# Kernel optimization log

Hardware: AMD Instinct MI355X
Metric: run time of the kernel (lower is better)

Reference implementation:

```python
import jax, jax.numpy as jnp
import numpy as np

D_MODEL = 1024
N_HEADS = 16
HEAD_DIM = D_MODEL // N_HEADS
D_FF = 4096
LN_EPS = 1e-5


def setup_inputs() -> dict:
    key = jax.random.key(0)
    ks = jax.random.split(key, 13)
    s = lambda fan_in: 1.0 / np.sqrt(fan_in)
    return {
        "x": jax.random.normal(ks[0], (2, 2048, D_MODEL), dtype=jnp.float32),
        "w_qkv": jax.random.uniform(ks[1], (D_MODEL, 3 * D_MODEL), jnp.float32, -s(D_MODEL), s(D_MODEL)),
        "b_qkv": jax.random.uniform(ks[2], (3 * D_MODEL,), jnp.float32, -s(D_MODEL), s(D_MODEL)),
        "w_out": jax.random.uniform(ks[3], (D_MODEL, D_MODEL), jnp.float32, -s(D_MODEL), s(D_MODEL)),
        "b_out": jax.random.uniform(ks[4], (D_MODEL,), jnp.float32, -s(D_MODEL), s(D_MODEL)),
        "w_ff1": jax.random.uniform(ks[5], (D_MODEL, D_FF), jnp.float32, -s(D_MODEL), s(D_MODEL)),
        "b_ff1": jax.random.uniform(ks[6], (D_FF,), jnp.float32, -s(D_MODEL), s(D_MODEL)),
        "w_ff2": jax.random.uniform(ks[7], (D_FF, D_MODEL), jnp.float32, -s(D_FF), s(D_FF)),
        "b_ff2": jax.random.uniform(ks[8], (D_MODEL,), jnp.float32, -s(D_FF), s(D_FF)),
        "ln1_g": jnp.ones((D_MODEL,), jnp.float32),
        "ln1_b": jnp.zeros((D_MODEL,), jnp.float32),
        "ln2_g": jnp.ones((D_MODEL,), jnp.float32),
        "ln2_b": jnp.zeros((D_MODEL,), jnp.float32),
    }


def _layer_norm(x, g, b):
    mu = jnp.mean(x, axis=-1, keepdims=True)
    var = jnp.mean(jnp.square(x - mu), axis=-1, keepdims=True)
    return (x - mu) * jax.lax.rsqrt(var + LN_EPS) * g + b


def reference(x, w_qkv, b_qkv, w_out, b_out, w_ff1, b_ff1, w_ff2, b_ff2,
              ln1_g, ln1_b, ln2_g, ln2_b):
    B, S, D = x.shape
    scale = HEAD_DIM ** -0.5
    qkv = x @ w_qkv + b_qkv                                   # [B,S,3D]
    qkv = qkv.reshape(B, S, 3, N_HEADS, HEAD_DIM)
    q, k, v = (qkv[:, :, 0], qkv[:, :, 1], qkv[:, :, 2])      # [B,S,H,Dh]
    attn = jnp.einsum("bqhd,bkhd->bhqk", q, k) * scale        # [B,H,S,S]
    attn = jax.nn.softmax(attn, axis=-1)
    o = jnp.einsum("bhqk,bkhd->bqhd", attn, v).reshape(B, S, D)
    o = o @ w_out + b_out
    x = _layer_norm(x + o, ln1_g, ln1_b)
    # FFN: Linear -> exact GELU -> Linear (dropout = 0)
    h = jax.nn.gelu(x @ w_ff1 + b_ff1, approximate=False)
    ff = h @ w_ff2 + b_ff2
    x = _layer_norm(x + ff, ln2_g, ln2_b)
    return x
```

## Files before the change

kernel.cpp:

```cpp
#include <hip/hip_runtime.h>
#include <hip/hip_bf16.h>
#include <cstdint>
#include <cstddef>

using bf16 = __hip_bfloat16;
typedef __attribute__((ext_vector_type(8))) short bf16x8;
typedef __attribute__((ext_vector_type(4))) float f32x4;

#define TOKENS 4096
#define DMODEL 1024
#define DFF    4096
#define SEQ    2048
#define NHEAD  16
#define HDIM   64
#define KVBLK  64
#define NT     (SEQ / KVBLK)
#define QSCALE 0.1803368801111f

__device__ __forceinline__ void async16(const void* g, void* l) {
  __builtin_amdgcn_global_load_lds(
      (const __attribute__((address_space(1))) void*)g,
      (__attribute__((address_space(3))) void*)l, 16, 0, 0);
}

__device__ __forceinline__ f32x4 mfma16(bf16x8 a, bf16x8 b, f32x4 c) {
  return __builtin_amdgcn_mfma_f32_16x16x32_bf16(a, b, c, 0, 0, 0);
}

__device__ __forceinline__ float exp2_fast(float x) {
  float r;
  asm("v_exp_f32 %0, %1" : "=v"(r) : "v"(x));
  return r;
}

__global__ void cast_bf16_k(const float* __restrict__ src, bf16* __restrict__ dst, int n) {
  int i = (blockIdx.x * blockDim.x + threadIdx.x) * 4;
  if (i >= n) return;
  float4 v = *(const float4*)(src + i);
  dst[i + 0] = __float2bfloat16(v.x);
  dst[i + 1] = __float2bfloat16(v.y);
  dst[i + 2] = __float2bfloat16(v.z);
  dst[i + 3] = __float2bfloat16(v.w);
}

__global__ void transpose_cast_k(const float* __restrict__ src, bf16* __restrict__ dst,
                                 int K, int N) {
  __shared__ float tile[32][33];
  int nt = blockIdx.x * 32, kt = blockIdx.y * 32;
  int tx = threadIdx.x, ty = threadIdx.y;
  #pragma unroll
  for (int i = 0; i < 32; i += 8)
    tile[ty + i][tx] = src[(size_t)(kt + ty + i) * N + nt + tx];
  __syncthreads();
  #pragma unroll
  for (int i = 0; i < 32; i += 8)
    dst[(size_t)(nt + ty + i) * K + kt + tx] = __float2bfloat16(tile[tx][ty + i]);
}

template <int EPI, int BN>
__global__ __launch_bounds__(256, 2)
void gemm_bt(const bf16* __restrict__ A, const bf16* __restrict__ Bt,
             const float* __restrict__ bias, int M, int N, int K,
             float* __restrict__ outf, bf16* __restrict__ outb,
             const float* __restrict__ resid,
             bf16* __restrict__ Qb, bf16* __restrict__ Kb, bf16* __restrict__ Vtb) {
  constexpr int MR = (BN == 128) ? 4 : 2;
  __shared__ bf16 Al[3][128 * 32];
  __shared__ bf16 Bl[3][BN * 32];
  const int t = threadIdx.x;
  const int nwg = gridDim.x * gridDim.y;
  const int flat = blockIdx.y * gridDim.x + blockIdx.x;
  const int swz = (flat & 7) * (nwg >> 3) + (flat >> 3);
  const int bm = (swz / gridDim.x) * 128, bn = (swz % gridDim.x) * BN;
  const int wid = t >> 6, lane = t & 63, g = lane >> 4, r = lane & 15;
  const int wr = (BN == 128) ? (wid >> 1) * 64 : wid * 32;
  const int wc = (BN == 128) ? (wid & 1) * 64 : 0;

  const f32x4 zero = {0.f, 0.f, 0.f, 0.f};
  f32x4 acc[MR][4];
  #pragma unroll
  for (int i = 0; i < MR; i++)
    #pragma unroll
    for (int j = 0; j < 4; j++) acc[i][j] = zero;

  const int ar0 = t >> 2, ac = (t & 3) * 8;
  const int ar1 = ar0 + 64;
  const int ach0 = t * 16, ach1 = ach0 + 4096;

  const int NK = K >> 5;
  #define STAGE(ktile, pb)                                                          \
    do {                                                                            \
      const int kk = (ktile) << 5;                                                  \
      async16(A + (size_t)(bm + ar0) * K + kk + ac, (char*)Al[pb] + ach0);          \
      async16(A + (size_t)(bm + ar1) * K + kk + ac, (char*)Al[pb] + ach1);          \
      async16(Bt + (size_t)(bn + ar0) * K + kk + ac, (char*)Bl[pb] + ach0);         \
      if constexpr (BN == 128)                                                      \
        async16(Bt + (size_t)(bn + ar1) * K + kk + ac, (char*)Bl[pb] + ach1);       \
    } while (0)

  STAGE(0, 0);
  STAGE(1, 1);

  int cur = 0, stg = 2;
  #pragma unroll 1
  for (int it = 0; it < NK; ++it) {
    if (it + 1 < NK) {
      if constexpr (BN == 128)
        asm volatile("s_waitcnt vmcnt(4)" ::: "memory");
      else
        asm volatile("s_waitcnt vmcnt(3)" ::: "memory");
    } else {
      asm volatile("s_waitcnt vmcnt(0)" ::: "memory");
    }
    __builtin_amdgcn_sched_barrier(0);
    __builtin_amdgcn_s_barrier();
    __builtin_amdgcn_sched_barrier(0);
    if (it + 2 < NK) STAGE(it + 2, stg);

    bf16x8 af[MR], bfr[4];
    #pragma unroll
    for (int mt = 0; mt < MR; mt++)
      af[mt] = *(const bf16x8*)&Al[cur][(wr + mt * 16 + r) * 32 + 8 * g];
    #pragma unroll
    for (int nt = 0; nt < 4; nt++)
      bfr[nt] = *(const bf16x8*)&Bl[cur][(wc + nt * 16 + r) * 32 + 8 * g];
    __builtin_amdgcn_s_setprio(1);
    #pragma unroll
    for (int mt = 0; mt < MR; mt++)
      #pragma unroll
      for (int nt = 0; nt < 4; nt++)
        acc[mt][nt] = mfma16(af[mt], bfr[nt], acc[mt][nt]);
    __builtin_amdgcn_s_setprio(0);
    cur = (cur == 2) ? 0 : cur + 1;
    stg = (stg == 2) ? 0 : stg + 1;
  }
  #undef STAGE

  #pragma unroll
  for (int nt = 0; nt < 4; nt++) {
    const int col = bn + wc + nt * 16 + r;
    const float bv = bias[col];
    #pragma unroll
    for (int mt = 0; mt < MR; mt++) {
      #pragma unroll
      for (int j = 0; j < 4; j++) {
        const int row = bm + wr + mt * 16 + 4 * g + j;
        float v = acc[mt][nt][j] + bv;
        if constexpr (EPI == 0) {
          const int part = col >> 10, hd = col & 1023, h = hd >> 6, d = hd & 63;
          const int b_ = row >> 11, s_ = row & 2047;
          if (part == 0) {
            Qb[((size_t)(b_ * NHEAD + h) * SEQ + s_) * HDIM + d] =
                __float2bfloat16(v * QSCALE);
          } else if (part == 1) {
            Kb[((size_t)(b_ * NHEAD + h) * SEQ + s_) * HDIM + d] = __float2bfloat16(v);
          } else {
            Vtb[((size_t)(b_ * NHEAD + h) * HDIM + d) * SEQ + s_] = __float2bfloat16(v);
          }
        } else if constexpr (EPI == 1) {
          const size_t idx = (size_t)row * N + col;
          outf[idx] = v + resid[idx];
        } else {
          const size_t idx = (size_t)row * N + col;
          outb[idx] = __float2bfloat16(0.5f * v * (1.f + erff(v * 0.70710678118f)));
        }
      }
    }
  }
}

__global__ __launch_bounds__(256, 4)
void attn_k(const bf16* __restrict__ Q, const bf16* __restrict__ Km,
            const bf16* __restrict__ Vt, bf16* __restrict__ O) {
  __shared__ bf16 Kl[2][KVBLK * 64];
  __shared__ bf16 Vl[2][KVBLK * 64];
  __shared__ bf16 P[4][16 * 64];
  const int b = blockIdx.x;
  const int bswz = (b & 7) * 128 + (b >> 3);
  const int bh = bswz >> 5, qb = bswz & 31;
  const int t = threadIdx.x, wid = t >> 6, lane = t & 63, g = lane >> 4, r = lane & 15;
  const int q0 = qb * 64 + wid * 16;
  const bf16* Qp = Q + (size_t)bh * SEQ * HDIM;
  const char* Kc = (const char*)(Km + (size_t)bh * SEQ * HDIM);
  const char* Vc = (const char*)(Vt + (size_t)bh * HDIM * SEQ);

  const bf16x8 qf0 = *(const bf16x8*)&Qp[(q0 + r) * HDIM + 8 * g];
  const bf16x8 qf1 = *(const bf16x8*)&Qp[(q0 + r) * HDIM + 8 * g + 32];

  const int o0 = wid * 2048 + lane * 16, o1 = o0 + 1024;
  const int cs0 = ((((o0 >> 4) & 7) ^ ((o0 >> 7) & 7)) << 4);
  const int cs1 = ((((o1 >> 4) & 7) ^ ((o1 >> 7) & 7)) << 4);
  const int kso0 = (o0 & ~127) + cs0, kso1 = (o1 & ~127) + cs1;
  const int vso0 = (o0 >> 7) * (SEQ * 2) + cs0, vso1 = (o1 >> 7) * (SEQ * 2) + cs1;

  const f32x4 zero = {0.f, 0.f, 0.f, 0.f};
  f32x4 oacc[4];
  #pragma unroll
  for (int i = 0; i < 4; i++) oacc[i] = zero;
  float mrow = -1e30f, lrow = 0.f;
  bf16* pl = P[wid];
  const int cA = ((g ^ (r & 7)) << 3), cB = (((g + 4) ^ (r & 7)) << 3);

  {
    char* kd = (char*)Kl[0]; char* vd = (char*)Vl[0];
    async16(Kc + kso0, kd + o0); async16(Kc + kso1, kd + o1);
    async16(Vc + vso0, vd + o0); async16(Vc + vso1, vd + o1);
  }

  #pragma unroll 1
  for (int tt = 0; tt < NT; ++tt) {
    if (tt + 1 < NT) {
      const char* ks = Kc + (tt + 1) * (KVBLK * HDIM * 2);
      const char* vs = Vc + (tt + 1) * (KVBLK * 2);
      char* kd = (char*)Kl[(tt + 1) & 1]; char* vd = (char*)Vl[(tt + 1) & 1];
      async16(ks + kso0, kd + o0); async16(ks + kso1, kd + o1);
      async16(vs + vso0, vd + o0); async16(vs + vso1, vd + o1);
      asm volatile("s_waitcnt vmcnt(4)" ::: "memory");
    } else {
      asm volatile("s_waitcnt vmcnt(0)" ::: "memory");
    }
    __builtin_amdgcn_sched_barrier(0);
    __builtin_amdgcn_s_barrier();
    __builtin_amdgcn_sched_barrier(0);

    const bf16* kbuf = Kl[tt & 1];
    const bf16* vbuf = Vl[tt & 1];

    f32x4 sacc[4];
    #pragma unroll
    for (int kt = 0; kt < 4; kt++) {
      const bf16* krow = kbuf + (kt * 16 + r) * 64;
      bf16x8 ka = *(const bf16x8*)&krow[cA];
      bf16x8 kb = *(const bf16x8*)&krow[cB];
      f32x4 s = zero;
      s = mfma16(ka, qf0, s);
      s = mfma16(kb, qf1, s);
      sacc[kt] = s;
    }

    float m0 = fmaxf(fmaxf(sacc[0][0], sacc[0][1]), fmaxf(sacc[0][2], sacc[0][3]));
    float m1 = fmaxf(fmaxf(sacc[1][0], sacc[1][1]), fmaxf(sacc[1][2], sacc[1][3]));
    float m2 = fmaxf(fmaxf(sacc[2][0], sacc[2][1]), fmaxf(sacc[2][2], sacc[2][3]));
    float m3 = fmaxf(fmaxf(sacc[3][0], sacc[3][1]), fmaxf(sacc[3][2], sacc[3][3]));
    float mx = fmaxf(fmaxf(m0, m1), fmaxf(m2, m3));
    mx = fmaxf(mx, __shfl_xor(mx, 16));
    mx = fmaxf(mx, __shfl_xor(mx, 32));
    const bool grow = !__all(mx <= mrow + 8.f);
    float corr = 1.f;
    if (grow) {
      const float mn = fmaxf(mrow, mx);
      corr = exp2_fast(mrow - mn);
      mrow = mn;
    }
    float sum = 0.f;
    float sv[4][4];
    #pragma unroll
    for (int kt = 0; kt < 4; kt++)
      #pragma unroll
      for (int j = 0; j < 4; j++) {
        const float p = exp2_fast(sacc[kt][j] - mrow);
        sv[kt][j] = p;
        sum += p;
      }
    sum += __shfl_xor(sum, 16);
    sum += __shfl_xor(sum, 32);
    lrow = lrow * corr + sum;

    #pragma unroll
    for (int kt = 0; kt < 4; kt++) {
      bf16 pk[4] = {__float2bfloat16(sv[kt][0]), __float2bfloat16(sv[kt][1]),
                    __float2bfloat16(sv[kt][2]), __float2bfloat16(sv[kt][3])};
      const int pc = (((kt * 2 + (g >> 1)) ^ (r & 7)) << 4) + ((g & 1) << 3);
      *(short4*)((char*)pl + r * 128 + pc) = *(const short4*)pk;
    }
    asm volatile("s_waitcnt lgkmcnt(0)" ::: "memory");
    __builtin_amdgcn_sched_barrier(0);
    const bf16x8 pf0 = *(const bf16x8*)((const char*)pl + r * 128 + (cA << 1));
    const bf16x8 pf1 = *(const bf16x8*)((const char*)pl + r * 128 + (cB << 1));

    if (grow) {
      float cq[4];
      #pragma unroll
      for (int j = 0; j < 4; j++) cq[j] = __shfl(corr, 4 * g + j);
      #pragma unroll
      for (int dt = 0; dt < 4; dt++)
        #pragma unroll
        for (int j = 0; j < 4; j++) oacc[dt][j] *= cq[j];
    }

    #pragma unroll
    for (int dt = 0; dt < 4; dt++) {
      const bf16* vrow = vbuf + (dt * 16 + r) * 64;
      bf16x8 v0 = *(const bf16x8*)&vrow[cA];
      bf16x8 v1 = *(const bf16x8*)&vrow[cB];
      oacc[dt] = mfma16(pf0, v0, oacc[dt]);
      oacc[dt] = mfma16(pf1, v1, oacc[dt]);
    }
    __builtin_amdgcn_sched_barrier(0);
    __builtin_amdgcn_s_barrier();
  }

  float lq[4];
  #pragma unroll
  for (int j = 0; j < 4; j++) lq[j] = __shfl(lrow, 4 * g + j);
  const int b_ = bh >> 4, h = bh & 15;
  #pragma unroll
  for (int dt = 0; dt < 4; dt++)
    #pragma unroll
    for (int j = 0; j < 4; j++) {
      const int tok = b_ * SEQ + q0 + 4 * g + j;
      O[(size_t)tok * DMODEL + h * HDIM + dt * 16 + r] =
          __float2bfloat16(oacc[dt][j] / lq[j]);
    }
}

__global__ __launch_bounds__(256)
void ln_k(const float* __restrict__ in, const float* __restrict__ gw,
          const float* __restrict__ bw, float* __restrict__ outf,
          bf16* __restrict__ outb) {
  const int row = blockIdx.x, t = threadIdx.x;
  const float4 v = *(const float4*)(in + (size_t)row * DMODEL + t * 4);
  float s = v.x + v.y + v.z + v.w;
  float s2 = v.x * v.x + v.y * v.y + v.z * v.z + v.w * v.w;
  #pragma unroll
  for (int m = 1; m < 64; m <<= 1) { s += __shfl_xor(s, m); s2 += __shfl_xor(s2, m); }
  __shared__ float red[8];
  const int wid = t >> 6, lane = t & 63;
  if (lane == 0) { red[wid] = s; red[4 + wid] = s2; }
  __syncthreads();
  s = red[0] + red[1] + red[2] + red[3];
  s2 = red[4] + red[5] + red[6] + red[7];
  const float mu = s * (1.f / DMODEL);
  const float rstd = rsqrtf(s2 * (1.f / DMODEL) - mu * mu + 1e-5f);
  const float4 gv = *(const float4*)(gw + t * 4);
  const float4 bv = *(const float4*)(bw + t * 4);
  float o0 = (v.x - mu) * rstd * gv.x + bv.x;
  float o1 = (v.y - mu) * rstd * gv.y + bv.y;
  float o2 = (v.z - mu) * rstd * gv.z + bv.z;
  float o3 = (v.w - mu) * rstd * gv.w + bv.w;
  if (outf) {
    float4 ov = {o0, o1, o2, o3};
    *(float4*)(outf + (size_t)row * DMODEL + t * 4) = ov;
  }
  if (outb) {
    bf16* p = outb + (size_t)row * DMODEL + t * 4;
    p[0] = __float2bfloat16(o0); p[1] = __float2bfloat16(o1);
    p[2] = __float2bfloat16(o2); p[3] = __float2bfloat16(o3);
  }
}

extern "C" void kernel_launch(void* const* d_in, const int* in_sizes, int n_in,
                              void* d_out, int out_size, void* d_ws, size_t ws_size,
                              hipStream_t stream) {
  const float* x     = (const float*)d_in[0];
  const float* w_qkv = (const float*)d_in[1];
  const float* b_qkv = (const float*)d_in[2];
  const float* w_out = (const float*)d_in[3];
  const float* b_out = (const float*)d_in[4];
  const float* w_ff1 = (const float*)d_in[5];
  const float* b_ff1 = (const float*)d_in[6];
  const float* w_ff2 = (const float*)d_in[7];
  const float* b_ff2 = (const float*)d_in[8];
  const float* ln1_g = (const float*)d_in[9];
  const float* ln1_b = (const float*)d_in[10];
  const float* ln2_g = (const float*)d_in[11];
  const float* ln2_b = (const float*)d_in[12];
  float* out = (float*)d_out;

  char* base = (char*)d_ws;
  bf16* wqkvT = (bf16*)(base);
  bf16* woutT = (bf16*)(base + 6291456);
  bf16* wff1T = (bf16*)(base + 8388608);
  bf16* wff2T = (bf16*)(base + 16777216);
  bf16* Qb    = (bf16*)(base + 25165824);
  bf16* Kb    = (bf16*)(base + 33554432);
  bf16* Vtb   = (bf16*)(base + 41943040);
  bf16* xob   = (bf16*)(base + 50331648);
  bf16* hb    = (bf16*)(base + 25165824);
  float* y    = (float*)(base + 58720256);
  float* x1f  = (float*)(base + 75497472);
  bf16* x1b   = (bf16*)(base + 92274688);
  (void)in_sizes; (void)n_in; (void)out_size; (void)ws_size;

  dim3 tb(32, 8);
  transpose_cast_k<<<dim3(3072 / 32, 1024 / 32), tb, 0, stream>>>(w_qkv, wqkvT, 1024, 3072);
  transpose_cast_k<<<dim3(1024 / 32, 1024 / 32), tb, 0, stream>>>(w_out, woutT, 1024, 1024);
  transpose_cast_k<<<dim3(4096 / 32, 1024 / 32), tb, 0, stream>>>(w_ff1, wff1T, 1024, 4096);
  transpose_cast_k<<<dim3(1024 / 32, 4096 / 32), tb, 0, stream>>>(w_ff2, wff2T, 4096, 1024);
  cast_bf16_k<<<(TOKENS * DMODEL / 4 + 255) / 256, 256, 0, stream>>>(x, xob, TOKENS * DMODEL);

  gemm_bt<0, 128><<<dim3(3072 / 128, TOKENS / 128), 256, 0, stream>>>(
      xob, wqkvT, b_qkv, TOKENS, 3072, 1024, nullptr, nullptr, nullptr, Qb, Kb, Vtb);
  attn_k<<<dim3(1024), 256, 0, stream>>>(Qb, Kb, Vtb, xob);
  gemm_bt<1, 64><<<dim3(1024 / 64, TOKENS / 128), 256, 0, stream>>>(
      xob, woutT, b_out, TOKENS, 1024, 1024, y, nullptr, x, nullptr, nullptr, nullptr);
  ln_k<<<TOKENS, 256, 0, stream>>>(y, ln1_g, ln1_b, x1f, x1b);
  gemm_bt<2, 128><<<dim3(4096 / 128, TOKENS / 128), 256, 0, stream>>>(
      x1b, wff1T, b_ff1, TOKENS, 4096, 1024, nullptr, hb, nullptr, nullptr, nullptr, nullptr);
  gemm_bt<1, 64><<<dim3(1024 / 64, TOKENS / 128), 256, 0, stream>>>(
      hb, wff2T, b_ff2, TOKENS, 1024, 4096, y, nullptr, x1f, nullptr, nullptr, nullptr);
  ln_k<<<TOKENS, 256, 0, stream>>>(y, ln2_g, ln2_b, out, nullptr);
}
```

Measured before the change: 304.3 us.

## Switch GEMM to double-buffered LDS pipeline and use fast approximate GELU

The GEMM goes from a three-stage async LDS pipeline to two stages. Each iteration now prefetches only the next tile and waits for all loads plus a barrier at the end. The setprio hints around the MFMA block are removed. Separately, exact erff in the GELU epilogue is replaced by an Abramowitz-Stegun polynomial erf using hardware rcp and exp2, which cuts epilogue math cost but adds roughly 1e-7 absolute erf error. The shallower pipeline reduces LDS use and may raise occupancy, but it exposes more global-load latency per k-step.

```diff
diff --git a/kernel.cpp b/kernel.cpp
--- a/kernel.cpp
+++ b/kernel.cpp
@@ -33,6 +33,20 @@
   return r;
 }
 
+__device__ __forceinline__ float gelu_fast(float x) {
+  const float z = fabsf(x) * 0.70710678118f;
+  const float t = __builtin_amdgcn_rcpf(1.f + 0.3275911f * z);
+  float p = 1.061405429f;
+  p = p * t - 1.453152027f;
+  p = p * t + 1.421413741f;
+  p = p * t - 0.284496736f;
+  p = p * t + 0.254829592f;
+  const float e = exp2_fast(-z * z * 1.44269504089f);
+  float erf = 1.f - p * t * e;
+  erf = (x < 0.f) ? -erf : erf;
+  return 0.5f * x * (1.f + erf);
+}
+
 __global__ void cast_bf16_k(const float* __restrict__ src, bf16* __restrict__ dst, int n) {
   int i = (blockIdx.x * blockDim.x + threadIdx.x) * 4;
   if (i >= n) return;
@@ -65,8 +79,8 @@
              const float* __restrict__ resid,
              bf16* __restrict__ Qb, bf16* __restrict__ Kb, bf16* __restrict__ Vtb) {
   constexpr int MR = (BN == 128) ? 4 : 2;
-  __shared__ bf16 Al[3][128 * 32];
-  __shared__ bf16 Bl[3][BN * 32];
+  __shared__ bf16 Al[2][128 * 32];
+  __shared__ bf16 Bl[2][BN * 32];
   const int t = threadIdx.x;
   const int nwg = gridDim.x * gridDim.y;
   const int flat = blockIdx.y * gridDim.x + blockIdx.x;
@@ -99,24 +113,13 @@
     } while (0)
 
   STAGE(0, 0);
-  STAGE(1, 1);
-
-  int cur = 0, stg = 2;
+  asm volatile("s_waitcnt vmcnt(0)" ::: "memory");
+  __builtin_amdgcn_s_barrier();
+
   #pragma unroll 1
   for (int it = 0; it < NK; ++it) {
-    if (it + 1 < NK) {
-      if constexpr (BN == 128)
-        asm volatile("s_waitcnt vmcnt(4)" ::: "memory");
-      else
-        asm volatile("s_waitcnt vmcnt(3)" ::: "memory");
-    } else {
-      asm volatile("s_waitcnt vmcnt(0)" ::: "memory");
-    }
-    __builtin_amdgcn_sched_barrier(0);
-    __builtin_amdgcn_s_barrier();
-    __builtin_amdgcn_sched_barrier(0);
-    if (it + 2 < NK) STAGE(it + 2, stg);
-
+    const int cur = it & 1;
+    if (it + 1 < NK) STAGE(it + 1, cur ^ 1);
     bf16x8 af[MR], bfr[4];
     #pragma unroll
     for (int mt = 0; mt < MR; mt++)
@@ -124,15 +127,14 @@
     #pragma unroll
     for (int nt = 0; nt < 4; nt++)
       bfr[nt] = *(const bf16x8*)&Bl[cur][(wc + nt * 16 + r) * 32 + 8 * g];
-    __builtin_amdgcn_s_setprio(1);
     #pragma unroll
     for (int mt = 0; mt < MR; mt++)
       #pragma unroll
       for (int nt = 0; nt < 4; nt++)
         acc[mt][nt] = mfma16(af[mt], bfr[nt], acc[mt][nt]);
-    __builtin_amdgcn_s_setprio(0);
-    cur = (cur == 2) ? 0 : cur + 1;
-    stg = (stg == 2) ? 0 : stg + 1;
+    __builtin_amdgcn_sched_barrier(0);
+    asm volatile("s_waitcnt vmcnt(0)" ::: "memory");
+    __builtin_amdgcn_s_barrier();
   }
   #undef STAGE
 
@@ -162,7 +164,7 @@
           outf[idx] = v + resid[idx];
         } else {
           const size_t idx = (size_t)row * N + col;
-          outb[idx] = __float2bfloat16(0.5f * v * (1.f + erff(v * 0.70710678118f)));
+          outb[idx] = __float2bfloat16(gelu_fast(v));
         }
       }
     }
```

New measurement: 279.4 us. -8.2%, faster.
